# Kernel tuning notes

Hardware: AMD Instinct MI355X
Metric: run time of the kernel (lower is better)

The kernel has to match this reference:

```python
import jax, jax.numpy as jnp
import numpy as np

B, K, D, N = 256, 1024, 2048, 50000
T = 0.07
MOMENTUM = 0.5
Z = 52580.0  # hardcoded partition-function constant from the source


def setup_inputs() -> dict:
    key = jax.random.key(0)
    k1, k2, k3, k4 = jax.random.split(key, 4)
    x = jax.random.normal(k1, (B, D), dtype=jnp.float32)  # encoder output (pre-normalize)
    y = jax.random.randint(k2, (B,), 0, N)
    idx = jax.random.randint(k3, (B, K), 0, N)
    stdv = 1.0 / np.sqrt(D / 3.0)
    memory = jax.random.uniform(k4, (N, D), dtype=jnp.float32, minval=-stdv, maxval=stdv)
    return {"x": x, "y": y, "idx": idx, "memory": memory}


def reference(x, y, idx, memory):
    # Normalize(2): L2-normalize features per row
    features = x / jnp.linalg.norm(x, axis=1, keepdims=True)  # [B, D]
    # idx.select(1, 0).copy_(y): positive index in column 0
    idx = idx.at[:, 0].set(y)
    # large random-index gather from the memory bank: [B, K, D]
    weight = jnp.take(memory, idx.reshape(-1), axis=0).reshape(B, K, D)
    # batched dot-product (bmm), temperature, exp, normalize by Z
    output = jnp.exp(jnp.einsum("bkd,bd->bk", weight, features) / T) / Z  # [B, K]
    # momentum update of the positive rows (uses pre-update weight[:, 0])
    weight_pos = weight[:, 0, :] * MOMENTUM + features * (1.0 - MOMENTUM)  # [B, D]
    updated = weight_pos / jnp.linalg.norm(weight_pos, axis=1, keepdims=True)
    # index_copy_ scatter back into a clone of the memory bank
    temp = memory.at[y].set(updated)  # [N, D]
    return output, temp
```

## Files before the change

### kernel.cpp

```cpp
#include <hip/hip_runtime.h>
#include <math.h>

#define NB 256
#define NK 1024
#define ND 2048
#define NN 50000

constexpr float T_INV = 1.0f / 0.07f;
constexpr float Z_INV = 1.0f / 52580.0f;
constexpr float MOM   = 0.5f;

__device__ __forceinline__ float blk_reduce_sum256(float v, float* sh) {
    #pragma unroll
    for (int o = 32; o > 0; o >>= 1) v += __shfl_down(v, o, 64);
    int lane = threadIdx.x & 63;
    int wid  = threadIdx.x >> 6;
    if (lane == 0) sh[wid] = v;
    __syncthreads();
    float s = sh[0] + sh[1] + sh[2] + sh[3];
    __syncthreads();
    return s;
}

__global__ void k_feat(const float* __restrict__ x, float* __restrict__ feat) {
    __shared__ float sh[4];
    int b = blockIdx.x;
    int t = threadIdx.x;
    const float4* xr = (const float4*)(x + (size_t)b * ND);
    float4 v0 = xr[t];
    float4 v1 = xr[t + 256];
    float ss = v0.x*v0.x + v0.y*v0.y + v0.z*v0.z + v0.w*v0.w
             + v1.x*v1.x + v1.y*v1.y + v1.z*v1.z + v1.w*v1.w;
    float s = blk_reduce_sum256(ss, sh);
    float r = rsqrtf(s);
    float4* fr = (float4*)(feat + (size_t)b * ND);
    fr[t]       = make_float4(v0.x*r, v0.y*r, v0.z*r, v0.w*r);
    fr[t + 256] = make_float4(v1.x*r, v1.y*r, v1.z*r, v1.w*r);
}

#define KPW 16
#define WPB 4
__global__ void k_dots(const float* __restrict__ mem, const float* __restrict__ feat,
                       const int* __restrict__ idx, const int* __restrict__ y,
                       float* __restrict__ out) {
    int wave = threadIdx.x >> 6;
    int lane = threadIdx.x & 63;
    const int bpb = NK / (KPW * WPB);
    int b  = blockIdx.x / bpb;
    int k0 = (blockIdx.x % bpb) * (KPW * WPB) + wave * KPW;

    const float4* f4 = (const float4*)(feat + (size_t)b * ND);
    float4 ff[8];
    #pragma unroll
    for (int j = 0; j < 8; ++j) ff[j] = f4[lane + 64 * j];

    const int* idxrow = idx + (size_t)b * NK;
    for (int i = 0; i < KPW; ++i) {
        int k = k0 + i;
        int row = (k == 0) ? y[b] : idxrow[k];
        const float4* m4 = (const float4*)(mem + (size_t)row * ND);
        float acc = 0.f;
        #pragma unroll
        for (int j = 0; j < 8; ++j) {
            float4 m = m4[lane + 64 * j];
            acc += m.x*ff[j].x + m.y*ff[j].y + m.z*ff[j].z + m.w*ff[j].w;
        }
        #pragma unroll
        for (int o = 32; o > 0; o >>= 1) acc += __shfl_down(acc, o, 64);
        if (lane == 0)
            out[(size_t)b * NK + k] = expf(acc * T_INV) * Z_INV;
    }
}

__global__ void k_copy(const float* __restrict__ mem, float* __restrict__ temp) {
    size_t i = (size_t)blockIdx.x * 256 + threadIdx.x;
    ((float4*)temp)[i] = ((const float4*)mem)[i];
}

__global__ void k_scatter(const float* __restrict__ mem, const float* __restrict__ feat,
                          const int* __restrict__ y, float* __restrict__ temp) {
    __shared__ float sh[4];
    int b  = blockIdx.x;
    int yb = y[b];
    for (int b2 = b + 1; b2 < NB; ++b2)
        if (y[b2] == yb) return;
    int t = threadIdx.x;
    const float4* f4 = (const float4*)(feat + (size_t)b * ND);
    const float4* m4 = (const float4*)(mem  + (size_t)yb * ND);
    float4 f0 = f4[t], f1 = f4[t + 256];
    float4 m0 = m4[t], m1 = m4[t + 256];
    float4 w0 = make_float4(m0.x*MOM + f0.x*(1.f-MOM), m0.y*MOM + f0.y*(1.f-MOM),
                            m0.z*MOM + f0.z*(1.f-MOM), m0.w*MOM + f0.w*(1.f-MOM));
    float4 w1 = make_float4(m1.x*MOM + f1.x*(1.f-MOM), m1.y*MOM + f1.y*(1.f-MOM),
                            m1.z*MOM + f1.z*(1.f-MOM), m1.w*MOM + f1.w*(1.f-MOM));
    float ss = w0.x*w0.x + w0.y*w0.y + w0.z*w0.z + w0.w*w0.w
             + w1.x*w1.x + w1.y*w1.y + w1.z*w1.z + w1.w*w1.w;
    float s = blk_reduce_sum256(ss, sh);
    float r = rsqrtf(s);
    float4* d = (float4*)(temp + (size_t)yb * ND);
    d[t]       = make_float4(w0.x*r, w0.y*r, w0.z*r, w0.w*r);
    d[t + 256] = make_float4(w1.x*r, w1.y*r, w1.z*r, w1.w*r);
}

extern "C" void kernel_launch(void* const* d_in, const int* in_sizes, int n_in,
                              void* d_out, int out_size, void* d_ws, size_t ws_size,
                              hipStream_t stream) {
    (void)in_sizes; (void)n_in; (void)out_size; (void)ws_size;
    const float* x   = (const float*)d_in[0];
    const int*   y   = (const int*)d_in[1];
    const int*   idx = (const int*)d_in[2];
    const float* mem = (const float*)d_in[3];

    float* out  = (float*)d_out;
    float* temp = (float*)d_out + (size_t)NB * NK;
    float* feat = (float*)d_ws;

    k_feat<<<NB, 256, 0, stream>>>(x, feat);
    k_dots<<<(NB * NK) / (KPW * WPB), 256, 0, stream>>>(mem, feat, idx, y, out);
    k_copy<<<(NN * ND / 4) / 256, 256, 0, stream>>>(mem, temp);
    k_scatter<<<NB, 256, 0, stream>>>(mem, feat, y, temp);
}
```

Before: 953.1 us.

## Replace per-pair gather dots with dense bf16 MFMA GEMM over memory bank

Instead of gathering B*K random memory rows and dotting each against its feature vector, this computes a dense score matrix memory x features^T for all N rows using bf16 MFMA, then gathers the needed scores in a small epilogue kernel. The memory bank is read once instead of 262K random row reads, and the clone copy into temp is fused into the GEMM's streaming loop. The change truncates memory values to bf16 (features round to nearest), which loses precision in the exponentiated logits. It also needs a large workspace for the N x B score matrix, with a fallback path that stages in the output buffer.

```diff
diff --git a/kernel.cpp b/kernel.cpp
--- a/kernel.cpp
+++ b/kernel.cpp
@@ -5,10 +5,15 @@
 #define NK 1024
 #define ND 2048
 #define NN 50000
+#define BM 64
 
 constexpr float T_INV = 1.0f / 0.07f;
 constexpr float Z_INV = 1.0f / 52580.0f;
 constexpr float MOM   = 0.5f;
+
+typedef float f32x4 __attribute__((ext_vector_type(4)));
+typedef short s16x8 __attribute__((ext_vector_type(8)));
+typedef unsigned int u32x4 __attribute__((ext_vector_type(4)));
 
 __device__ __forceinline__ float blk_reduce_sum256(float v, float* sh) {
     #pragma unroll
@@ -22,7 +27,13 @@
     return s;
 }
 
-__global__ void k_feat(const float* __restrict__ x, float* __restrict__ feat) {
+__device__ __forceinline__ unsigned f2bf_rne(float f) {
+    unsigned u = __float_as_uint(f);
+    return (u + 0x7fffu + ((u >> 16) & 1u)) >> 16;
+}
+
+__global__ void k_feat(const float* __restrict__ x, float* __restrict__ feat,
+                       unsigned int* __restrict__ featb) {
     __shared__ float sh[4];
     int b = blockIdx.x;
     int t = threadIdx.x;
@@ -33,43 +44,101 @@
              + v1.x*v1.x + v1.y*v1.y + v1.z*v1.z + v1.w*v1.w;
     float s = blk_reduce_sum256(ss, sh);
     float r = rsqrtf(s);
+    v0.x*=r; v0.y*=r; v0.z*=r; v0.w*=r;
+    v1.x*=r; v1.y*=r; v1.z*=r; v1.w*=r;
     float4* fr = (float4*)(feat + (size_t)b * ND);
-    fr[t]       = make_float4(v0.x*r, v0.y*r, v0.z*r, v0.w*r);
-    fr[t + 256] = make_float4(v1.x*r, v1.y*r, v1.z*r, v1.w*r);
-}
-
-#define KPW 16
-#define WPB 4
-__global__ void k_dots(const float* __restrict__ mem, const float* __restrict__ feat,
-                       const int* __restrict__ idx, const int* __restrict__ y,
-                       float* __restrict__ out) {
-    int wave = threadIdx.x >> 6;
-    int lane = threadIdx.x & 63;
-    const int bpb = NK / (KPW * WPB);
-    int b  = blockIdx.x / bpb;
-    int k0 = (blockIdx.x % bpb) * (KPW * WPB) + wave * KPW;
-
-    const float4* f4 = (const float4*)(feat + (size_t)b * ND);
-    float4 ff[8];
-    #pragma unroll
-    for (int j = 0; j < 8; ++j) ff[j] = f4[lane + 64 * j];
-
-    const int* idxrow = idx + (size_t)b * NK;
-    for (int i = 0; i < KPW; ++i) {
-        int k = k0 + i;
-        int row = (k == 0) ? y[b] : idxrow[k];
-        const float4* m4 = (const float4*)(mem + (size_t)row * ND);
-        float acc = 0.f;
-        #pragma unroll
-        for (int j = 0; j < 8; ++j) {
-            float4 m = m4[lane + 64 * j];
-            acc += m.x*ff[j].x + m.y*ff[j].y + m.z*ff[j].z + m.w*ff[j].w;
+    fr[t]       = v0;
+    fr[t + 256] = v1;
+    unsigned int* fb = featb + (size_t)b * (ND / 2);
+    fb[2*t]           = f2bf_rne(v0.x) | (f2bf_rne(v0.y) << 16);
+    fb[2*t + 1]       = f2bf_rne(v0.z) | (f2bf_rne(v0.w) << 16);
+    fb[2*(t+256)]     = f2bf_rne(v1.x) | (f2bf_rne(v1.y) << 16);
+    fb[2*(t+256) + 1] = f2bf_rne(v1.z) | (f2bf_rne(v1.w) << 16);
+}
+
+template<bool COPY>
+__launch_bounds__(256)
+__global__ void k_gemm(const float* __restrict__ mem, const short* __restrict__ featb,
+                       float* __restrict__ S, float* __restrict__ temp) {
+    const int wave = threadIdx.x >> 6;
+    const int lane = threadIdx.x & 63;
+    const int rlo  = lane & 15;
+    const int khi  = lane >> 4;
+    const int n0   = blockIdx.x * BM;
+
+    const float* aptr[4];
+    #pragma unroll
+    for (int m = 0; m < 4; ++m) {
+        int r = n0 + m * 16 + rlo;
+        if (r >= NN) r = NN - 1;
+        aptr[m] = mem + (size_t)r * ND + khi * 8;
+    }
+    const short* bptr[4];
+    #pragma unroll
+    for (int j = 0; j < 4; ++j) {
+        int c = wave * 64 + j * 16 + rlo;
+        bptr[j] = featb + (size_t)c * ND + khi * 8;
+    }
+    const int crow = n0 + (threadIdx.x >> 2);
+    const int ccol = (threadIdx.x & 3) * 8;
+    const bool cok = COPY && (crow < NN);
+    const float4* csrc = (const float4*)(mem  + (size_t)crow * ND + ccol);
+    float4*       cdst = (float4*)(temp + (size_t)crow * ND + ccol);
+
+    f32x4 acc[4][4] = {};
+
+    for (int k0 = 0; k0 < ND; k0 += 32) {
+        s16x8 bfr[4];
+        #pragma unroll
+        for (int j = 0; j < 4; ++j)
+            bfr[j] = *(const s16x8*)(bptr[j] + k0);
+        s16x8 afr[4];
+        #pragma unroll
+        for (int m = 0; m < 4; ++m) {
+            const float* p = aptr[m] + k0;
+            float4 x0 = *(const float4*)p;
+            float4 x1 = *(const float4*)(p + 4);
+            u32x4 uv = { (__float_as_uint(x0.x) >> 16) | (__float_as_uint(x0.y) & 0xffff0000u),
+                         (__float_as_uint(x0.z) >> 16) | (__float_as_uint(x0.w) & 0xffff0000u),
+                         (__float_as_uint(x1.x) >> 16) | (__float_as_uint(x1.y) & 0xffff0000u),
+                         (__float_as_uint(x1.z) >> 16) | (__float_as_uint(x1.w) & 0xffff0000u) };
+            afr[m] = __builtin_bit_cast(s16x8, uv);
         }
         #pragma unroll
-        for (int o = 32; o > 0; o >>= 1) acc += __shfl_down(acc, o, 64);
-        if (lane == 0)
-            out[(size_t)b * NK + k] = expf(acc * T_INV) * Z_INV;
-    }
+        for (int m = 0; m < 4; ++m)
+            #pragma unroll
+            for (int j = 0; j < 4; ++j)
+                acc[m][j] = __builtin_amdgcn_mfma_f32_16x16x32_bf16(afr[m], bfr[j], acc[m][j], 0, 0, 0);
+        if (cok) {
+            cdst[k0 / 4]     = csrc[k0 / 4];
+            cdst[k0 / 4 + 1] = csrc[k0 / 4 + 1];
+        }
+    }
+
+    const int r_off = (lane >> 4) * 4;
+    const int c_off = lane & 15;
+    #pragma unroll
+    for (int m = 0; m < 4; ++m) {
+        int row0 = n0 + m * 16 + r_off;
+        #pragma unroll
+        for (int j = 0; j < 4; ++j) {
+            int col = wave * 64 + j * 16 + c_off;
+            #pragma unroll
+            for (int r = 0; r < 4; ++r) {
+                int row = row0 + r;
+                if (row < NN) S[(size_t)row * NB + col] = acc[m][j][r];
+            }
+        }
+    }
+}
+
+__global__ void k_out(const float* __restrict__ S, const int* __restrict__ idx,
+                      const int* __restrict__ y, float* __restrict__ out) {
+    int g = blockIdx.x * 256 + threadIdx.x;
+    int b = g >> 10;
+    int k = g & (NK - 1);
+    int row = (k == 0) ? y[b] : idx[g];
+    out[g] = expf(S[(size_t)row * NB + b] * T_INV) * Z_INV;
 }
 
 __global__ void k_copy(const float* __restrict__ mem, float* __restrict__ temp) {
@@ -105,7 +174,7 @@
 extern "C" void kernel_launch(void* const* d_in, const int* in_sizes, int n_in,
                               void* d_out, int out_size, void* d_ws, size_t ws_size,
                               hipStream_t stream) {
-    (void)in_sizes; (void)n_in; (void)out_size; (void)ws_size;
+    (void)in_sizes; (void)n_in; (void)out_size;
     const float* x   = (const float*)d_in[0];
     const int*   y   = (const int*)d_in[1];
     const int*   idx = (const int*)d_in[2];
@@ -113,10 +182,28 @@
 
     float* out  = (float*)d_out;
     float* temp = (float*)d_out + (size_t)NB * NK;
-    float* feat = (float*)d_ws;
-
-    k_feat<<<NB, 256, 0, stream>>>(x, feat);
-    k_dots<<<(NB * NK) / (KPW * WPB), 256, 0, stream>>>(mem, feat, idx, y, out);
-    k_copy<<<(NN * ND / 4) / 256, 256, 0, stream>>>(mem, temp);
-    k_scatter<<<NB, 256, 0, stream>>>(mem, feat, y, temp);
-}
+
+    const size_t szF  = (size_t)NB * ND * sizeof(float);
+    const size_t szFB = (size_t)NB * ND * sizeof(short);
+    const size_t szS  = (size_t)NN * NB * sizeof(float);
+    const int gemm_grid = (NN + BM - 1) / BM;
+
+    if (ws_size >= szF + szFB + szS) {
+        float*        feat  = (float*)d_ws;
+        unsigned int* featb = (unsigned int*)((char*)d_ws + szF);
+        float*        S     = (float*)((char*)d_ws + szF + szFB);
+        k_feat<<<NB, 256, 0, stream>>>(x, feat, featb);
+        k_gemm<true><<<gemm_grid, 256, 0, stream>>>(mem, (const short*)featb, S, temp);
+        k_out<<<(NB * NK) / 256, 256, 0, stream>>>(S, idx, y, out);
+        k_scatter<<<NB, 256, 0, stream>>>(mem, feat, y, temp);
+    } else {
+        float*        feat  = (float*)d_ws;
+        unsigned int* featb = (unsigned int*)temp;
+        float*        S     = (float*)((char*)temp + szFB);
+        k_feat<<<NB, 256, 0, stream>>>(x, feat, featb);
+        k_gemm<false><<<gemm_grid, 256, 0, stream>>>(mem, (const short*)featb, S, nullptr);
+        k_out<<<(NB * NK) / 256, 256, 0, stream>>>(S, idx, y, out);
+        k_copy<<<(NN * ND / 4) / 256, 256, 0, stream>>>(mem, temp);
+        k_scatter<<<NB, 256, 0, stream>>>(mem, feat, y, temp);
+    }
+}
```

Result: slower. 1.002 ms (+5.1%).
